# Optimization experiments

Measured on AMD Instinct MI355X. Metric: run time of the kernel, lower is better.

## Reference

```python
import jax, jax.numpy as jnp
import numpy as np
import math

N_HEADS = 12
K1 = 20
K2 = 20


def _pair(hidden, mask4, H, k1, k2):
    # hidden: [b, L, D]; mask4: [b, 1, L, L]
    b, L, D = hidden.shape
    d = D // H
    h = hidden.reshape(b, L, H, d).transpose(0, 2, 1, 3)  # [b,H,L,d]
    scores = jnp.einsum('bhid,bhjd->bhij', h, h) / math.sqrt(d)  # [b,H,L,L]
    scores = scores * mask4
    att = jax.nn.softmax(scores + (1.0 - mask4) * -10000.0, axis=-1) * mask4
    g_score = att.sum(axis=(1, 2))  # [b,L]
    _, g_top = jax.lax.top_k(g_score, k1)  # [b,k1]
    loc = att.sum(axis=1) * (1.0 - jnp.eye(L, dtype=att.dtype))  # zero diagonal
    _, l_top = jax.lax.top_k(loc, k2)  # [b,L,k2]
    idx = jnp.broadcast_to(g_top[:, :, None], (b, k1, k2))
    l_top = jnp.take_along_axis(l_top, idx, axis=1)  # [b,k1,k2]
    return scores, g_top, l_top


def _triplet(hidden, mask, g_top, l_top):
    # hidden: [b,L,D]; mask: [b,L]; g_top: [b,k1]; l_top: [b,k1,k2]; n_heads=1
    b, L, D = hidden.shape
    k1, k2 = l_top.shape[1], l_top.shape[2]
    h = hidden[:, None]  # [b,1,L,D]
    idx1 = jnp.broadcast_to(g_top[:, None, :, None], (b, 1, k1, D))
    h1 = jnp.take_along_axis(h, idx1, axis=2)  # [b,1,k1,D]
    sd = h1[:, :, :, None, :] - h[:, :, None, :, :]  # [b,1,k1,L,D]
    idx2 = jnp.broadcast_to(l_top[:, None, :, :, None], (b, 1, k1, k2, D))
    sd = jnp.take_along_axis(sd, idx2, axis=3)  # [b,1,k1,k2,D]
    nrm = jnp.linalg.norm(sd, axis=-1, keepdims=True)
    nsd = sd / jnp.maximum(nrm, 1e-12)  # F.normalize(p=2, eps=1e-12)
    angle = jnp.einsum('bhijd,bhikd->bhijk', nsd, nsd)  # [b,1,k1,k2,k2]
    m1 = jnp.take_along_axis(mask, g_top, axis=1)  # [b,k1]
    me = (m1[:, :, None] + mask[:, None, :])[:, None, :, :, None]  # [b,1,k1,L,1]
    idx3 = jnp.broadcast_to(l_top[:, None, :, :, None], (b, 1, k1, k2, 1))
    me = jnp.take_along_axis(me, idx3, axis=3)  # [b,1,k1,k2,1]
    amask = (me * me.swapaxes(-2, -1) == 4.0).astype(angle.dtype)  # both valid
    nz = (angle != 0).astype(angle.dtype) * (1.0 - jnp.eye(k2, dtype=angle.dtype))
    amask = amask * nz
    return angle * amask, amask


def setup_inputs() -> dict:
    key = jax.random.key(0)
    k1, k2 = jax.random.split(key)
    b, L, D = 8, 512, 768
    return {
        's_rep': jax.random.normal(k1, (b, L, D), dtype=jnp.float32),
        't_rep': jax.random.normal(k2, (b, L, D), dtype=jnp.float32),
        'attention_mask': jnp.ones((b, L), dtype=jnp.float32),
    }


def reference(s_rep, t_rep, attention_mask):
    b, L, D = s_rep.shape
    k1 = min(K1, L)
    k2 = min(K2, L)
    mext = attention_mask[:, :, None] * attention_mask[:, None, :]  # [b,L,L]
    mask4 = mext[:, None, :, :]  # broadcasts over heads
    s_pair, s_g, s_l = _pair(s_rep, mask4, N_HEADS, k1, k2)
    t_rep_ng = jax.lax.stop_gradient(t_rep)
    t_pair, t_g, t_l = _pair(t_rep_ng, mask4, N_HEADS, k1, k2)
    t_pair = jax.lax.stop_gradient(t_pair)
    denom = N_HEADS * jnp.sum(mext)
    loss_pair = jnp.sum((s_pair - t_pair) ** 2) / denom
    s_angle, s_mask = _triplet(s_rep, attention_mask, t_g, t_l)
    t_angle, t_mask = _triplet(t_rep_ng, attention_mask, t_g, t_l)
    t_angle = jax.lax.stop_gradient(t_angle)
    diff = s_angle - t_angle
    ad = jnp.abs(diff)
    sl1 = jnp.where(ad < 1.0, 0.5 * diff * diff, ad - 0.5)  # smooth_l1, beta=1
    loss_triplet = jnp.sum(sl1) / jnp.sum(s_mask)
    return loss_pair + loss_triplet
```

## Files before the change

kernel.cpp:

```cpp
#include <hip/hip_runtime.h>
#include <hip/hip_bf16.h>
#include <math.h>

#define Bn 8
#define Ln 512
#define Dn 768
#define NHn 12
#define DHn 64
#define K1n 20
#define K2n 20
#define BST 72
#define TROWS 64

#define WS_ACC    0
#define WS_GSCORE 64
#define WS_GTOP   16448
#define WS_LOCP   17152
#define WS_SBF    3949312
#define WS_TBF    10240768

typedef __attribute__((ext_vector_type(8))) short bf16x8;
typedef __attribute__((ext_vector_type(4))) float f32x4;

__device__ inline unsigned short f2bf(float x) {
  __hip_bfloat16 h = __float2bfloat16(x);
  return *reinterpret_cast<unsigned short*>(&h);
}
__device__ inline float bf2f(unsigned short u) {
  return __uint_as_float(((unsigned int)u) << 16);
}

__global__ __launch_bounds__(256) void prep_bf16_kernel(
    const float* __restrict__ s, const float* __restrict__ t,
    unsigned short* __restrict__ sbf, unsigned short* __restrict__ tbf,
    float* __restrict__ g_score, int* __restrict__ accw) {
  int tid = threadIdx.x;
  if (blockIdx.x == 0) {
    if (tid < 16) accw[tid] = 0;
    for (int i = tid; i < Bn * Ln; i += 256) g_score[i] = 0.0f;
  }
  int gid = blockIdx.x * 256 + tid;
  int f = gid * 4;
  int col = f % Dn;
  int rb = f / Dn;
  int row = rb & (Ln - 1);
  int b = rb >> 9;
  int h = col >> 6;
  int k = col & 63;
  size_t dst = (((size_t)(b * NHn + h) * Ln + row) * DHn + k);
  float4 vs = *(const float4*)(s + f);
  float4 vt = *(const float4*)(t + f);
  ushort4 us, ut;
  us.x = f2bf(vs.x); us.y = f2bf(vs.y); us.z = f2bf(vs.z); us.w = f2bf(vs.w);
  ut.x = f2bf(vt.x); ut.y = f2bf(vt.y); ut.z = f2bf(vt.z); ut.w = f2bf(vt.w);
  *(ushort4*)(sbf + dst) = us;
  *(ushort4*)(tbf + dst) = ut;
}

__global__ __launch_bounds__(256) void pairA_kernel(
    const unsigned short* __restrict__ sbf, const unsigned short* __restrict__ tbf,
    const float* __restrict__ mask, float* __restrict__ g_score,
    double* __restrict__ acc) {
  const int b = blockIdx.x & 7;
  const int r = blockIdx.x >> 3;
  const int it = r / NHn;
  const int h = r - it * NHn;
  const int tid = threadIdx.x;
  const int w = tid >> 6;
  const int lane = tid & 63;
  const int lr = lane & 15, lg = lane >> 4;

  __shared__ unsigned short Bs[2][TROWS * BST];
  __shared__ unsigned short Bt[2][TROWS * BST];
  __shared__ float Mcol[Ln];
  __shared__ float gcol[Ln];
  __shared__ float wred[4];

  const int s_r0 = tid >> 3;
  const int s_r1 = s_r0 + 32;
  const int s_c = (tid & 7) * 8;

  for (int j = tid; j < Ln; j += 256) {
    Mcol[j] = mask[b * Ln + j];
    gcol[j] = 0.0f;
  }

  const size_t hb = (size_t)(b * NHn + h) * Ln;
  const int rw = it * 64 + w * 16;
  const unsigned short* pas = sbf + (hb + rw + lr) * DHn + lg * 8;
  const unsigned short* pat = tbf + (hb + rw + lr) * DHn + lg * 8;
  bf16x8 sa0 = *(const bf16x8*)pas;
  bf16x8 sa1 = *(const bf16x8*)(pas + 32);
  bf16x8 ta0 = *(const bf16x8*)pat;
  bf16x8 ta1 = *(const bf16x8*)(pat + 32);

  {
    bf16x8 v0 = *(const bf16x8*)(sbf + (hb + s_r0) * DHn + s_c);
    bf16x8 v1 = *(const bf16x8*)(sbf + (hb + s_r1) * DHn + s_c);
    bf16x8 u0 = *(const bf16x8*)(tbf + (hb + s_r0) * DHn + s_c);
    bf16x8 u1 = *(const bf16x8*)(tbf + (hb + s_r1) * DHn + s_c);
    *(bf16x8*)&Bs[0][s_r0 * BST + s_c] = v0;
    *(bf16x8*)&Bs[0][s_r1 * BST + s_c] = v1;
    *(bf16x8*)&Bt[0][s_r0 * BST + s_c] = u0;
    *(bf16x8*)&Bt[0][s_r1 * BST + s_c] = u1;
  }
  __syncthreads();

  float mrow[4];
  #pragma unroll
  for (int q = 0; q < 4; ++q) mrow[q] = Mcol[rw + lg * 4 + q];

  const f32x4 zero4 = {0.0f, 0.0f, 0.0f, 0.0f};
  float lpair = 0.0f;
  float rsum[4] = {0.0f, 0.0f, 0.0f, 0.0f};

  #pragma unroll 1
  for (int t = 0; t < 8; ++t) {
    const int cur = t & 1;
    bf16x8 v0, v1, u0, u1;
    if (t < 7) {
      const int jn = (t + 1) * TROWS;
      v0 = *(const bf16x8*)(sbf + (hb + jn + s_r0) * DHn + s_c);
      v1 = *(const bf16x8*)(sbf + (hb + jn + s_r1) * DHn + s_c);
      u0 = *(const bf16x8*)(tbf + (hb + jn + s_r0) * DHn + s_c);
      u1 = *(const bf16x8*)(tbf + (hb + jn + s_r1) * DHn + s_c);
    }
    #pragma unroll
    for (int c = 0; c < 4; ++c) {
      const int jl = c * 16;
      const int j0 = t * TROWS + jl;
      const unsigned short* pbs = &Bs[cur][(jl + lr) * BST + lg * 8];
      const unsigned short* pbt = &Bt[cur][(jl + lr) * BST + lg * 8];
      bf16x8 sb0 = *(const bf16x8*)pbs;
      bf16x8 sb1 = *(const bf16x8*)(pbs + 32);
      bf16x8 tb0 = *(const bf16x8*)pbt;
      bf16x8 tb1 = *(const bf16x8*)(pbt + 32);
      f32x4 sacc = __builtin_amdgcn_mfma_f32_16x16x32_bf16(sa0, sb0, zero4, 0, 0, 0);
      sacc = __builtin_amdgcn_mfma_f32_16x16x32_bf16(sa1, sb1, sacc, 0, 0, 0);
      f32x4 tacc = __builtin_amdgcn_mfma_f32_16x16x32_bf16(ta0, tb0, zero4, 0, 0, 0);
      tacc = __builtin_amdgcn_mfma_f32_16x16x32_bf16(ta1, tb1, tacc, 0, 0, 0);
      const float mj = Mcol[j0 + lr];
      #pragma unroll
      for (int q = 0; q < 4; ++q) {
        const float mm = mrow[q] * mj;
        const float ss = sacc[q] * 0.125f * mm;
        const float st = tacc[q] * 0.125f * mm;
        const float d = ss - st;
        lpair += d * d;
        rsum[q] += __expf(st + (1.0f - mm) * (-10000.0f));
      }
    }
    if (t < 7) {
      const int nxt = cur ^ 1;
      *(bf16x8*)&Bs[nxt][s_r0 * BST + s_c] = v0;
      *(bf16x8*)&Bs[nxt][s_r1 * BST + s_c] = v1;
      *(bf16x8*)&Bt[nxt][s_r0 * BST + s_c] = u0;
      *(bf16x8*)&Bt[nxt][s_r1 * BST + s_c] = u1;
    }
    __syncthreads();
  }

  #pragma unroll
  for (int o = 1; o < 16; o <<= 1) {
    #pragma unroll
    for (int q = 0; q < 4; ++q) rsum[q] += __shfl_xor(rsum[q], o, 64);
  }
  float rscale[4];
  #pragma unroll
  for (int q = 0; q < 4; ++q)
    rscale[q] = mrow[q] / fmaxf(rsum[q], 1e-30f);

  {
    bf16x8 u0 = *(const bf16x8*)(tbf + (hb + s_r0) * DHn + s_c);
    bf16x8 u1 = *(const bf16x8*)(tbf + (hb + s_r1) * DHn + s_c);
    *(bf16x8*)&Bt[0][s_r0 * BST + s_c] = u0;
    *(bf16x8*)&Bt[0][s_r1 * BST + s_c] = u1;
  }
  __syncthreads();

  #pragma unroll 1
  for (int t = 0; t < 8; ++t) {
    const int cur = t & 1;
    bf16x8 u0, u1;
    if (t < 7) {
      const int jn = (t + 1) * TROWS;
      u0 = *(const bf16x8*)(tbf + (hb + jn + s_r0) * DHn + s_c);
      u1 = *(const bf16x8*)(tbf + (hb + jn + s_r1) * DHn + s_c);
    }
    #pragma unroll
    for (int c = 0; c < 4; ++c) {
      const int jl = c * 16;
      const int j0 = t * TROWS + jl;
      const unsigned short* pbt = &Bt[cur][(jl + lr) * BST + lg * 8];
      bf16x8 tb0 = *(const bf16x8*)pbt;
      bf16x8 tb1 = *(const bf16x8*)(pbt + 32);
      f32x4 tacc = __builtin_amdgcn_mfma_f32_16x16x32_bf16(ta0, tb0, zero4, 0, 0, 0);
      tacc = __builtin_amdgcn_mfma_f32_16x16x32_bf16(ta1, tb1, tacc, 0, 0, 0);
      const float mj = Mcol[j0 + lr];
      float pc = 0.0f;
      #pragma unroll
      for (int q = 0; q < 4; ++q) {
        const float mm = mrow[q] * mj;
        const float st = tacc[q] * 0.125f * mm;
        const float e = __expf(st + (1.0f - mm) * (-10000.0f));
        pc += e * rscale[q];
      }
      pc += __shfl_xor(pc, 16, 64);
      pc += __shfl_xor(pc, 32, 64);
      if (lg == 0) atomicAdd(&gcol[j0 + lr], pc);
    }
    if (t < 7) {
      const int nxt = cur ^ 1;
      *(bf16x8*)&Bt[nxt][s_r0 * BST + s_c] = u0;
      *(bf16x8*)&Bt[nxt][s_r1 * BST + s_c] = u1;
    }
    __syncthreads();
  }

  #pragma unroll
  for (int o = 1; o < 64; o <<= 1) lpair += __shfl_xor(lpair, o, 64);
  if (lane == 0) wred[w] = lpair;
  __syncthreads();

  if (tid == 0) {
    atomicAdd(&acc[0], (double)((wred[0] + wred[1]) + (wred[2] + wred[3])));
  }
  {
    const int j0 = tid, j1 = tid + 256;
    atomicAdd(&g_score[b * Ln + j0], gcol[j0] * Mcol[j0]);
    atomicAdd(&g_score[b * Ln + j1], gcol[j1] * Mcol[j1]);
  }
}

__global__ __launch_bounds__(256, 4) void pairB_kernel(
    const unsigned short* __restrict__ tbf, const float* __restrict__ mask,
    const float* __restrict__ g_score, int* __restrict__ g_top,
    float* __restrict__ loc_part) {
  const int b = blockIdx.x & 7;
  const int h = blockIdx.x >> 3;
  const int tid = threadIdx.x;
  const int w = tid >> 6, lane = tid & 63;
  const int lr = lane & 15, lg = lane >> 4;
  const int cw = w * 128;

  __shared__ int gidx[32];
  __shared__ float mrow_s[32];
  __shared__ float rscale_s[32];
  __shared__ float redsum[4][32];
  __shared__ float McolB[Ln];
  __shared__ unsigned short es[32][Ln + 8];

  for (int j = tid; j < Ln; j += 256) McolB[j] = mask[b * Ln + j];
  if (w == 1 && lane < 32 - K1n) gidx[K1n + lane] = 0;
  if (w == 0) {
    float v[8];
    #pragma unroll
    for (int q = 0; q < 8; ++q) v[q] = g_score[b * Ln + q * 64 + lane];
    for (int r = 0; r < K1n; ++r) {
      float bv = v[0]; int bq = 0;
      #pragma unroll
      for (int q = 1; q < 8; ++q) if (v[q] > bv) { bv = v[q]; bq = q; }
      int bj = bq * 64 + lane;
      #pragma unroll
      for (int o = 1; o < 64; o <<= 1) {
        float ov = __shfl_xor(bv, o, 64);
        int oj = __shfl_xor(bj, o, 64);
        if (ov > bv || (ov == bv && oj < bj)) { bv = ov; bj = oj; }
      }
      if (lane == 0) {
        gidx[r] = bj;
        if (h == 0) g_top[b * K1n + r] = bj;
      }
      const int wq = bj >> 6, wl = bj & 63;
      #pragma unroll
      for (int q = 0; q < 8; ++q)
        if (q == wq && lane == wl) v[q] = -3.0e38f;
    }
  }
  __syncthreads();
  if (tid < 32) mrow_s[tid] = (tid < K1n) ? McolB[gidx[tid]] : 0.0f;
  __syncthreads();

  const size_t hb = (size_t)(b * NHn + h) * Ln;
  bf16x8 ta[2][2];
  #pragma unroll
  for (int rt = 0; rt < 2; ++rt) {
    const unsigned short* p = tbf + (hb + gidx[rt * 16 + lr]) * DHn + lg * 8;
    ta[rt][0] = *(const bf16x8*)p;
    ta[rt][1] = *(const bf16x8*)(p + 32);
  }
  const f32x4 zero4 = {0.0f, 0.0f, 0.0f, 0.0f};
  float rsum[2][4] = {{0, 0, 0, 0}, {0, 0, 0, 0}};
  #pragma unroll 1
  for (int ct = 0; ct < 8; ++ct) {
    const int j0 = cw + ct * 16;
    const unsigned short* pb = tbf + (hb + j0 + lr) * DHn + lg * 8;
    bf16x8 tb0 = *(const bf16x8*)pb;
    bf16x8 tb1 = *(const bf16x8*)(pb + 32);
    const float mj = McolB[j0 + lr];
    #pragma unroll
    for (int rt = 0; rt < 2; ++rt) {
      f32x4 tacc = __builtin_amdgcn_mfma_f32_16x16x32_bf16(ta[rt][0], tb0, zero4, 0, 0, 0);
      tacc = __builtin_amdgcn_mfma_f32_16x16x32_bf16(ta[rt][1], tb1, tacc, 0, 0, 0);
      #pragma unroll
      for (int q = 0; q < 4; ++q) {
        const int ri = rt * 16 + lg * 4 + q;
        const float mm = mrow_s[ri] * mj;
        const float st = tacc[q] * 0.125f * mm;
        const float e = __expf(st + (1.0f - mm) * (-10000.0f));
        rsum[rt][q] += e;
        es[ri][j0 + lr] = f2bf(e);
      }
    }
  }
  #pragma unroll
  for (int o = 1; o < 16; o <<= 1) {
    #pragma unroll
    for (int rt = 0; rt < 2; ++rt)
      #pragma unroll
      for (int q = 0; q < 4; ++q) rsum[rt][q] += __shfl_xor(rsum[rt][q], o, 64);
  }
  if (lr == 0) {
    #pragma unroll
    for (int rt = 0; rt < 2; ++rt)
      #pragma unroll
      for (int q = 0; q < 4; ++q) redsum[w][rt * 16 + lg * 4 + q] = rsum[rt][q];
  }
  __syncthreads();
  if (tid < 32) {
    const float fs = redsum[0][tid] + redsum[1][tid] + redsum[2][tid] + redsum[3][tid];
    rscale_s[tid] = mrow_s[tid] / fmaxf(fs, 1e-30f);
  }
  __syncthreads();
  float* lp = loc_part + (size_t)(h * Bn + b) * K1n * Ln;
  for (int idx = tid; idx < K1n * Ln; idx += 256) {
    const int ri = idx >> 9, j = idx & (Ln - 1);
    const float e = bf2f(es[ri][j]);
    lp[idx] = e * rscale_s[ri] * McolB[j];
  }
}

#define TP (Dn + 16)

__global__ __launch_bounds__(256, 1) void triplet_kernel(
    const float* __restrict__ s_rep, const float* __restrict__ t_rep,
    const float* __restrict__ mask, const int* __restrict__ g_top,
    const float* __restrict__ loc_part, double* __restrict__ acc,
    unsigned int* __restrict__ done_cnt, float* __restrict__ out) {
  const int blk = blockIdx.x, tid = threadIdx.x;
  const int b = blk / K1n, i1 = blk % K1n;
  const int w = tid >> 6, lane = tid & 63;
  const int lr = lane & 15, lg = lane >> 4;

  __shared__ unsigned short NS[32][TP];
  __shared__ unsigned short NT[32][TP];
  __shared__ int lidx[K2n];
  __shared__ float fl2[K2n];
  __shared__ float sred[4], cred[4];
  __shared__ int is_last;
  __shared__ float red[4];

  const int g = g_top[b * K1n + i1];
  if (w == 0) {
    const float* r0 = loc_part + (size_t)(b * K1n + i1) * Ln;
    float v[8];
    #pragma unroll
    for (int q = 0; q < 8; ++q) {
      const int j = q * 64 + lane;
      float sv = 0.0f;
      #pragma unroll
      for (int hh = 0; hh < NHn; ++hh)
        sv += r0[(size_t)hh * Bn * K1n * Ln + j];
      v[q] = (j == g) ? 0.0f : sv;
    }
    for (int r = 0; r < K2n; ++r) {
      float bv = v[0]; int bq = 0;
      #pragma unroll
      for (int q = 1; q < 8; ++q) if (v[q] > bv) { bv = v[q]; bq = q; }
      int bj = bq * 64 + lane;
      #pragma unroll
      for (int o = 1; o < 64; o <<= 1) {
        float ov = __shfl_xor(bv, o, 64);
        int oj = __shfl_xor(bj, o, 64);
        if (ov > bv || (ov == bv && oj < bj)) { bv = ov; bj = oj; }
      }
      if (lane == 0) lidx[r] = bj;
      const int wq = bj >> 6, wl = bj & 63;
      #pragma unroll
      for (int q = 0; q < 8; ++q)
        if (q == wq && lane == wl) v[q] = -3.0e38f;
    }
  }
  __syncthreads();
  if (tid < K2n)
    fl2[tid] = (mask[b * Ln + g] + mask[b * Ln + lidx[tid]] == 2.0f) ? 1.0f : 0.0f;
  __syncthreads();

  const float* pgs = s_rep + (size_t)(b * Ln + g) * Dn;
  const float* pgt = t_rep + (size_t)(b * Ln + g) * Dn;
  for (int j = w; j < K2n; j += 4) {
    const float* pls = s_rep + (size_t)(b * Ln + lidx[j]) * Dn;
    const float* plt = t_rep + (size_t)(b * Ln + lidx[j]) * Dn;
    float4 ds[3], dt[3];
    float ssq = 0.0f, tsq = 0.0f;
    #pragma unroll
    for (int q = 0; q < 3; ++q) {
      const int c = lane * 4 + q * 256;
      float4 a = *(const float4*)&pgs[c];
      float4 x = *(const float4*)&pls[c];
      ds[q] = make_float4(a.x - x.x, a.y - x.y, a.z - x.z, a.w - x.w);
      ssq += ds[q].x * ds[q].x + ds[q].y * ds[q].y + ds[q].z * ds[q].z + ds[q].w * ds[q].w;
      float4 c2 = *(const float4*)&pgt[c];
      float4 y = *(const float4*)&plt[c];
      dt[q] = make_float4(c2.x - y.x, c2.y - y.y, c2.z - y.z, c2.w - y.w);
      tsq += dt[q].x * dt[q].x + dt[q].y * dt[q].y + dt[q].z * dt[q].z + dt[q].w * dt[q].w;
    }
    #pragma unroll
    for (int o = 1; o < 64; o <<= 1) {
      ssq += __shfl_xor(ssq, o, 64);
      tsq += __shfl_xor(tsq, o, 64);
    }
    const float sinv = 1.0f / fmaxf(sqrtf(ssq), 1e-12f);
    const float tinv = 1.0f / fmaxf(sqrtf(tsq), 1e-12f);
    #pragma unroll
    for (int q = 0; q < 3; ++q) {
      const int c = lane * 4 + q * 256;
      ushort4 us, ut;
      us.x = f2bf(ds[q].x * sinv); us.y = f2bf(ds[q].y * sinv);
      us.z = f2bf(ds[q].z * sinv); us.w = f2bf(ds[q].w * sinv);
      ut.x = f2bf(dt[q].x * tinv); ut.y = f2bf(dt[q].y * tinv);
      ut.z = f2bf(dt[q].z * tinv); ut.w = f2bf(dt[q].w * tinv);
      *(ushort4*)&NS[j][c] = us;
      *(ushort4*)&NT[j][c] = ut;
    }
  }
  __syncthreads();

  const int qr = w >> 1, qc = w & 1;
  f32x4 sacc = {0.0f, 0.0f, 0.0f, 0.0f};
  f32x4 tacc = {0.0f, 0.0f, 0.0f, 0.0f};
  #pragma unroll
  for (int ks = 0; ks < 24; ++ks) {
    const int kk = ks * 32 + lg * 8;
    bf16x8 as = *(const bf16x8*)&NS[qr * 16 + lr][kk];
    bf16x8 bs = *(const bf16x8*)&NS[qc * 16 + lr][kk];
    bf16x8 at = *(const bf16x8*)&NT[qr * 16 + lr][kk];
    bf16x8 bt = *(const bf16x8*)&NT[qc * 16 + lr][kk];
    sacc = __builtin_amdgcn_mfma_f32_16x16x32_bf16(as, bs, sacc, 0, 0, 0);
    tacc = __builtin_amdgcn_mfma_f32_16x16x32_bf16(at, bt, tacc, 0, 0, 0);
  }
  float psum = 0.0f, pcnt = 0.0f;
  #pragma unroll
  for (int q = 0; q < 4; ++q) {
    const int j2 = qr * 16 + lg * 4 + q;
    const int k2 = qc * 16 + lr;
    if (j2 < K2n && k2 < K2n && j2 != k2) {
      const float am = fl2[j2] * fl2[k2];
      const bool smv = (am != 0.0f) && (sacc[q] != 0.0f);
      const bool tmv = (am != 0.0f) && (tacc[q] != 0.0f);
      const float sv = smv ? sacc[q] : 0.0f;
      const float tv = tmv ? tacc[q] : 0.0f;
      const float d = sv - tv;
      const float ad = fabsf(d);
      psum += (ad < 1.0f) ? 0.5f * d * d : (ad - 0.5f);
      pcnt += smv ? 1.0f : 0.0f;
    }
  }
  #pragma unroll
  for (int o = 1; o < 64; o <<= 1) {
    psum += __shfl_xor(psum, o, 64);
    pcnt += __shfl_xor(pcnt, o, 64);
  }
  if (lane == 0) { sred[w] = psum; cred[w] = pcnt; }
  __syncthreads();
  if (tid == 0) {
    atomicAdd(&acc[1], (double)(sred[0] + sred[1] + sred[2] + sred[3]));
    atomicAdd(&acc[2], (double)(cred[0] + cred[1] + cred[2] + cred[3]));
    __threadfence();
    const unsigned int done = atomicAdd(done_cnt, 1u);
    is_last = (done == (unsigned int)(Bn * K1n - 1)) ? 1 : 0;
  }
  __syncthreads();

  if (is_last) {
    double sm = 0.0;
    for (int bb = 0; bb < Bn; ++bb) {
      float p = 0.0f;
      for (int i = tid; i < Ln; i += 256) p += mask[bb * Ln + i];
      #pragma unroll
      for (int o = 1; o < 64; o <<= 1) p += __shfl_xor(p, o, 64);
      __syncthreads();
      if ((tid & 63) == 0) red[tid >> 6] = p;
      __syncthreads();
      if (tid == 0) {
        float rs = red[0] + red[1] + red[2] + red[3];
        sm += (double)rs * (double)rs;
      }
    }
    __syncthreads();
    if (tid == 0) {
      const double a0 = atomicAdd(&acc[0], 0.0);
      const double a1 = atomicAdd(&acc[1], 0.0);
      const double a2 = atomicAdd(&acc[2], 0.0);
      const double lp = a0 / ((double)NHn * sm);
      const double lt = a1 / a2;
      out[0] = (float)(lp + lt);
    }
  }
}

extern "C" void kernel_launch(void* const* d_in, const int* in_sizes, int n_in,
                              void* d_out, int out_size, void* d_ws, size_t ws_size,
                              hipStream_t stream) {
  const float* s_rep = (const float*)d_in[0];
  const float* t_rep = (const float*)d_in[1];
  const float* mask  = (const float*)d_in[2];
  float* out = (float*)d_out;

  char* w = (char*)d_ws;
  double* acc      = (double*)(w + WS_ACC);
  unsigned int* done_cnt = (unsigned int*)(w + WS_ACC + 48);
  float* g_score   = (float*)(w + WS_GSCORE);
  int* g_top       = (int*)(w + WS_GTOP);
  float* loc_part  = (float*)(w + WS_LOCP);
  unsigned short* sbf = (unsigned short*)(w + WS_SBF);
  unsigned short* tbf = (unsigned short*)(w + WS_TBF);

  prep_bf16_kernel<<<Bn * Ln * Dn / 4 / 256, 256, 0, stream>>>(
      s_rep, t_rep, sbf, tbf, g_score, (int*)(w + WS_ACC));
  pairA_kernel<<<Bn * NHn * (Ln / 64), 256, 0, stream>>>(sbf, tbf, mask, g_score, acc);
  pairB_kernel<<<Bn * NHn, 256, 0, stream>>>(tbf, mask, g_score, g_top, loc_part);
  triplet_kernel<<<Bn * K1n, 256, 0, stream>>>(s_rep, t_rep, mask, g_top, loc_part,
                                               acc, done_cnt, out);
}
```

Measured before the change: 103.2 us.

## Widen triplet kernel to 512 threads with parallel head-sum and staged anchor rows

The triplet kernel now runs with 512 threads. The 12-head sum of the local-attention row is spread across all threads into shared memory instead of being done by one wave. The anchor rows of s and t are staged into shared memory once. The angle MFMAs are split so each of the 8 waves computes one 16x16 tile for either s or t, with results written to a shared Gram matrix and a flat 400-thread loss pass. This targets the serial head-sum and the under-used waves in this small 160-block kernel, at the cost of more shared memory and an extra barrier.

```diff
diff --git a/kernel.cpp b/kernel.cpp
--- a/kernel.cpp
+++ b/kernel.cpp
@@ -340,9 +340,9 @@
   }
 }
 
-#define TP (Dn + 16)
-
-__global__ __launch_bounds__(256, 1) void triplet_kernel(
+#define TPW (Dn + 16)
+
+__global__ __launch_bounds__(512, 1) void triplet_kernel(
     const float* __restrict__ s_rep, const float* __restrict__ t_rep,
     const float* __restrict__ mask, const int* __restrict__ g_top,
     const float* __restrict__ loc_part, double* __restrict__ acc,
@@ -352,27 +352,43 @@
   const int w = tid >> 6, lane = tid & 63;
   const int lr = lane & 15, lg = lane >> 4;
 
-  __shared__ unsigned short NS[32][TP];
-  __shared__ unsigned short NT[32][TP];
+  __shared__ unsigned short NS[32][TPW];
+  __shared__ unsigned short NT[32][TPW];
+  __shared__ float locsum[Ln];
+  __shared__ float gsr[Dn], gtr[Dn];
+  __shared__ float G[2][K2n][K2n + 1];
   __shared__ int lidx[K2n];
   __shared__ float fl2[K2n];
-  __shared__ float sred[4], cred[4];
+  __shared__ float sred[8], cred[8];
   __shared__ int is_last;
-  __shared__ float red[4];
+  __shared__ float red[8];
 
   const int g = g_top[b * K1n + i1];
+
+  {
+    const int j = tid;
+    float sv = 0.0f;
+    #pragma unroll
+    for (int hh = 0; hh < NHn; ++hh)
+      sv += loc_part[((size_t)(hh * Bn + b) * K1n + i1) * Ln + j];
+    locsum[j] = (j == g) ? 0.0f : sv;
+  }
+  {
+    const float* pgs = s_rep + (size_t)(b * Ln + g) * Dn;
+    const float* pgt = t_rep + (size_t)(b * Ln + g) * Dn;
+    if (tid < 192) {
+      *(float4*)&gsr[tid * 4] = *(const float4*)&pgs[tid * 4];
+    } else if (tid < 384) {
+      const int q4 = tid - 192;
+      *(float4*)&gtr[q4 * 4] = *(const float4*)&pgt[q4 * 4];
+    }
+  }
+  __syncthreads();
+
   if (w == 0) {
-    const float* r0 = loc_part + (size_t)(b * K1n + i1) * Ln;
     float v[8];
     #pragma unroll
-    for (int q = 0; q < 8; ++q) {
-      const int j = q * 64 + lane;
-      float sv = 0.0f;
-      #pragma unroll
-      for (int hh = 0; hh < NHn; ++hh)
-        sv += r0[(size_t)hh * Bn * K1n * Ln + j];
-      v[q] = (j == g) ? 0.0f : sv;
-    }
+    for (int q = 0; q < 8; ++q) v[q] = locsum[q * 64 + lane];
     for (int r = 0; r < K2n; ++r) {
       float bv = v[0]; int bq = 0;
       #pragma unroll
@@ -394,11 +410,8 @@
   __syncthreads();
   if (tid < K2n)
     fl2[tid] = (mask[b * Ln + g] + mask[b * Ln + lidx[tid]] == 2.0f) ? 1.0f : 0.0f;
-  __syncthreads();
-
-  const float* pgs = s_rep + (size_t)(b * Ln + g) * Dn;
-  const float* pgt = t_rep + (size_t)(b * Ln + g) * Dn;
-  for (int j = w; j < K2n; j += 4) {
+
+  for (int j = w; j < K2n; j += 8) {
     const float* pls = s_rep + (size_t)(b * Ln + lidx[j]) * Dn;
     const float* plt = t_rep + (size_t)(b * Ln + lidx[j]) * Dn;
     float4 ds[3], dt[3];
@@ -406,11 +419,11 @@
     #pragma unroll
     for (int q = 0; q < 3; ++q) {
       const int c = lane * 4 + q * 256;
-      float4 a = *(const float4*)&pgs[c];
+      float4 a = *(const float4*)&gsr[c];
       float4 x = *(const float4*)&pls[c];
       ds[q] = make_float4(a.x - x.x, a.y - x.y, a.z - x.z, a.w - x.w);
       ssq += ds[q].x * ds[q].x + ds[q].y * ds[q].y + ds[q].z * ds[q].z + ds[q].w * ds[q].w;
-      float4 c2 = *(const float4*)&pgt[c];
+      float4 c2 = *(const float4*)&gtr[c];
       float4 y = *(const float4*)&plt[c];
       dt[q] = make_float4(c2.x - y.x, c2.y - y.y, c2.z - y.z, c2.w - y.w);
       tsq += dt[q].x * dt[q].x + dt[q].y * dt[q].y + dt[q].z * dt[q].z + dt[q].w * dt[q].w;
@@ -436,34 +449,43 @@
   }
   __syncthreads();
 
-  const int qr = w >> 1, qc = w & 1;
-  f32x4 sacc = {0.0f, 0.0f, 0.0f, 0.0f};
-  f32x4 tacc = {0.0f, 0.0f, 0.0f, 0.0f};
-  #pragma unroll
-  for (int ks = 0; ks < 24; ++ks) {
-    const int kk = ks * 32 + lg * 8;
-    bf16x8 as = *(const bf16x8*)&NS[qr * 16 + lr][kk];
-    bf16x8 bs = *(const bf16x8*)&NS[qc * 16 + lr][kk];
-    bf16x8 at = *(const bf16x8*)&NT[qr * 16 + lr][kk];
-    bf16x8 bt = *(const bf16x8*)&NT[qc * 16 + lr][kk];
-    sacc = __builtin_amdgcn_mfma_f32_16x16x32_bf16(as, bs, sacc, 0, 0, 0);
-    tacc = __builtin_amdgcn_mfma_f32_16x16x32_bf16(at, bt, tacc, 0, 0, 0);
-  }
+  {
+    const int ts = w & 1;
+    const int qr = w >> 2;
+    const int qc = (w >> 1) & 1;
+    const unsigned short (*N)[TPW] = ts ? NT : NS;
+    f32x4 acc4 = {0.0f, 0.0f, 0.0f, 0.0f};
+    #pragma unroll
+    for (int ks = 0; ks < 24; ++ks) {
+      const int kk = ks * 32 + lg * 8;
+      bf16x8 a8 = *(const bf16x8*)&N[qr * 16 + lr][kk];
+      bf16x8 b8 = *(const bf16x8*)&N[qc * 16 + lr][kk];
+      acc4 = __builtin_amdgcn_mfma_f32_16x16x32_bf16(a8, b8, acc4, 0, 0, 0);
+    }
+    #pragma unroll
+    for (int q = 0; q < 4; ++q) {
+      const int j2 = qr * 16 + lg * 4 + q;
+      const int k2 = qc * 16 + lr;
+      if (j2 < K2n && k2 < K2n) G[ts][j2][k2] = acc4[q];
+    }
+  }
+  __syncthreads();
+
   float psum = 0.0f, pcnt = 0.0f;
-  #pragma unroll
-  for (int q = 0; q < 4; ++q) {
-    const int j2 = qr * 16 + lg * 4 + q;
-    const int k2 = qc * 16 + lr;
-    if (j2 < K2n && k2 < K2n && j2 != k2) {
+  if (tid < K2n * K2n) {
+    const int j2 = tid / K2n, k2 = tid - j2 * K2n;
+    if (j2 != k2) {
       const float am = fl2[j2] * fl2[k2];
-      const bool smv = (am != 0.0f) && (sacc[q] != 0.0f);
-      const bool tmv = (am != 0.0f) && (tacc[q] != 0.0f);
-      const float sv = smv ? sacc[q] : 0.0f;
-      const float tv = tmv ? tacc[q] : 0.0f;
+      const float sv0 = G[0][j2][k2];
+      const float tv0 = G[1][j2][k2];
+      const bool smv = (am != 0.0f) && (sv0 != 0.0f);
+      const bool tmv = (am != 0.0f) && (tv0 != 0.0f);
+      const float sv = smv ? sv0 : 0.0f;
+      const float tv = tmv ? tv0 : 0.0f;
       const float d = sv - tv;
       const float ad = fabsf(d);
-      psum += (ad < 1.0f) ? 0.5f * d * d : (ad - 0.5f);
-      pcnt += smv ? 1.0f : 0.0f;
+      psum = (ad < 1.0f) ? 0.5f * d * d : (ad - 0.5f);
+      pcnt = smv ? 1.0f : 0.0f;
     }
   }
   #pragma unroll
@@ -474,8 +496,11 @@
   if (lane == 0) { sred[w] = psum; cred[w] = pcnt; }
   __syncthreads();
   if (tid == 0) {
-    atomicAdd(&acc[1], (double)(sred[0] + sred[1] + sred[2] + sred[3]));
-    atomicAdd(&acc[2], (double)(cred[0] + cred[1] + cred[2] + cred[3]));
+    float ps = 0.0f, pcs = 0.0f;
+    #pragma unroll
+    for (int i = 0; i < 8; ++i) { ps += sred[i]; pcs += cred[i]; }
+    atomicAdd(&acc[1], (double)ps);
+    atomicAdd(&acc[2], (double)pcs);
     __threadfence();
     const unsigned int done = atomicAdd(done_cnt, 1u);
     is_last = (done == (unsigned int)(Bn * K1n - 1)) ? 1 : 0;
@@ -485,15 +510,16 @@
   if (is_last) {
     double sm = 0.0;
     for (int bb = 0; bb < Bn; ++bb) {
-      float p = 0.0f;
-      for (int i = tid; i < Ln; i += 256) p += mask[bb * Ln + i];
+      float p = (tid < Ln) ? mask[bb * Ln + tid] : 0.0f;
       #pragma unroll
       for (int o = 1; o < 64; o <<= 1) p += __shfl_xor(p, o, 64);
       __syncthreads();
       if ((tid & 63) == 0) red[tid >> 6] = p;
       __syncthreads();
       if (tid == 0) {
-        float rs = red[0] + red[1] + red[2] + red[3];
+        float rs = 0.0f;
+        #pragma unroll
+        for (int i = 0; i < 8; ++i) rs += red[i];
         sm += (double)rs * (double)rs;
       }
     }
@@ -530,6 +556,6 @@
       s_rep, t_rep, sbf, tbf, g_score, (int*)(w + WS_ACC));
   pairA_kernel<<<Bn * NHn * (Ln / 64), 256, 0, stream>>>(sbf, tbf, mask, g_score, acc);
   pairB_kernel<<<Bn * NHn, 256, 0, stream>>>(tbf, mask, g_score, g_top, loc_part);
-  triplet_kernel<<<Bn * K1n, 256, 0, stream>>>(s_rep, t_rep, mask, g_top, loc_part,
+  triplet_kernel<<<Bn * K1n, 512, 0, stream>>>(s_rep, t_rep, mask, g_top, loc_part,
                                                acc, done_cnt, out);
 }
```

Result: faster. 100.2 us (-3.0%).
